# Kernel tuning notes

Hardware: AMD Instinct MI355X
Metric: run time of the kernel (lower is better)

Reference implementation:

```python
import jax, jax.numpy as jnp
import numpy as np

N, E, L = 50000, 800000, 3
EPS = 1e-5


def mlp2(h, W1, b1, W2, b2):
    # Linear -> ReLU -> Linear
    return jax.nn.relu(h @ W1 + b1) @ W2 + b2


def setup_inputs() -> dict:
    key = jax.random.key(0)
    ks = jax.random.split(key, 20)
    s = 0.1  # weight scale to keep activations well-conditioned
    return {
        "x": jax.random.normal(ks[0], (N, 128), jnp.float32),
        "edge_attr": jax.random.normal(ks[1], (E, 64), jnp.float32),
        "edge_index": jax.random.randint(ks[2], (2, E), 0, N, dtype=jnp.int32),
        "Wn1": jax.random.normal(ks[3], (L, 128, 256), jnp.float32) * s,
        "bn1": jnp.zeros((L, 256), jnp.float32),
        "Wn2": jax.random.normal(ks[4], (L, 256, 128), jnp.float32) * s,
        "bn2": jnp.zeros((L, 128), jnp.float32),
        "We1": jax.random.normal(ks[5], (L, 64, 128), jnp.float32) * s,
        "be1": jnp.zeros((L, 128), jnp.float32),
        "We2": jax.random.normal(ks[6], (L, 128, 64), jnp.float32) * s,
        "be2": jnp.zeros((L, 64), jnp.float32),
        "Wm1": jax.random.normal(ks[7], (L, 320, 128), jnp.float32) * s,
        "bm1": jnp.zeros((L, 128), jnp.float32),
        "Wm2": jax.random.normal(ks[8], (L, 128, 128), jnp.float32) * s,
        "bm2": jnp.zeros((L, 128), jnp.float32),
        "lnw": jnp.ones((L, 128), jnp.float32),
        "lnb": jnp.zeros((L, 128), jnp.float32),
        "Wf": jax.random.normal(ks[9], (128, 64), jnp.float32) * s,
        "bf": jnp.zeros((64,), jnp.float32),
    }


def reference(x, edge_attr, edge_index, Wn1, bn1, Wn2, bn2, We1, be1, We2, be2,
              Wm1, bm1, Wm2, bm2, lnw, lnb, Wf, bf):
    src, dst = edge_index[0], edge_index[1]  # x_j = x[src], x_i = x[dst] (PyG source_to_target)
    deg = jax.ops.segment_sum(jnp.ones((E,), x.dtype), dst, num_segments=N)
    denom = jnp.maximum(deg, 1.0)[:, None]  # scatter-mean with clamp for isolated nodes
    for l in range(L):
        # mlp_node is the same function for x_i and x_j -> apply once per node, then gather
        xn = mlp2(x, Wn1[l], bn1[l], Wn2[l], bn2[l])        # [N, 128]
        e = mlp2(edge_attr, We1[l], be1[l], We2[l], be2[l])  # [E, 64]
        m = jnp.concatenate([xn[dst], xn[src], e], axis=-1)  # [E, 320] = [x_i, x_j, edge_attr]
        m = mlp2(m, Wm1[l], bm1[l], Wm2[l], bm2[l])          # [E, 128]
        agg = jax.ops.segment_sum(m, dst, num_segments=N) / denom  # mean aggregate [N, 128]
        mu = agg.mean(-1, keepdims=True)
        var = agg.var(-1, keepdims=True)
        h = (agg - mu) * jax.lax.rsqrt(var + EPS) * lnw[l] + lnb[l]  # LayerNorm
        x = jax.nn.relu(h)  # dropout p=0.0 -> identity
    return x @ Wf + bf  # jk='last' -> final linear on last layer output
```

## Files before the change

### kernel.cpp

```cpp
#include <hip/hip_runtime.h>
#include <stdint.h>

#define NN 50000
#define NE 800000
#define NB 196

typedef float f32x4 __attribute__((ext_vector_type(4)));
typedef short bf16x8 __attribute__((ext_vector_type(8)));

__device__ __forceinline__ unsigned short f2bf(float f) {
  union { float f; unsigned u; } v; v.f = f;
  unsigned r = v.u + 0x7fffu + ((v.u >> 16) & 1u);
  return (unsigned short)(r >> 16);
}
__device__ __forceinline__ float bf2f(unsigned short h) {
  union { unsigned u; float f; } v; v.u = ((unsigned)h) << 16;
  return v.f;
}
__device__ __forceinline__ float ldf(const void* p, size_t i, int m32) {
  return m32 ? ((const float*)p)[i] : bf2f(((const unsigned short*)p)[i]);
}

__global__ void detect_kernel(const void* lnw, int* flag) {
  if (threadIdx.x == 0 && blockIdx.x == 0)
    *flag = (((const unsigned short*)lnw)[0] == 0x3F80) ? 0 : 1;
}

#define oWn1 0
#define oWn2 98304
#define oWm1 196608
#define oWe1 319488
#define oWe2 344064
#define oWm2 368640
#define oWf  417792
#define NWTOT 425984
#define obn1 0
#define obn2 768
#define obe1 1152
#define obe2 1536
#define obm1 1728
#define obm2 2112
#define olnw 2496
#define olnb 2880
#define obf  3264
#define NBTOT 3328

__global__ __launch_bounds__(256) void conv_w(
    const void* Wn1, const void* Wn2, const void* Wm1, const void* We1,
    const void* We2, const void* Wm2, const void* Wf,
    const int* __restrict__ flg, unsigned short* __restrict__ cW)
{
  const int m32 = *flg;
  int i = blockIdx.x * 256 + threadIdx.x;
  if (i >= NWTOT) return;
  const void* src; size_t j;
  if      (i < oWn2) { src = Wn1; j = i - oWn1; }
  else if (i < oWm1) { src = Wn2; j = i - oWn2; }
  else if (i < oWe1) { src = Wm1; j = i - oWm1; }
  else if (i < oWe2) { src = We1; j = i - oWe1; }
  else if (i < oWm2) { src = We2; j = i - oWe2; }
  else if (i < oWf)  { src = Wm2; j = i - oWm2; }
  else               { src = Wf;  j = i - oWf;  }
  cW[i] = f2bf(ldf(src, j, m32));
}

__global__ __launch_bounds__(256) void conv_b(
    const void* bn1, const void* bn2, const void* be1, const void* be2,
    const void* bm1, const void* bm2, const void* lnw, const void* lnb,
    const void* bfv, const int* __restrict__ flg, float* __restrict__ cB)
{
  const int m32 = *flg;
  int i = blockIdx.x * 256 + threadIdx.x;
  if (i >= NBTOT) return;
  const void* src; size_t j;
  if      (i < obn2) { src = bn1; j = i - obn1; }
  else if (i < obe1) { src = bn2; j = i - obn2; }
  else if (i < obe2) { src = be1; j = i - obe1; }
  else if (i < obm1) { src = be2; j = i - obe2; }
  else if (i < obm2) { src = bm1; j = i - obm1; }
  else if (i < olnw) { src = bm2; j = i - obm2; }
  else if (i < olnb) { src = lnw; j = i - olnw; }
  else if (i < obf)  { src = lnb; j = i - olnb; }
  else               { src = bfv; j = i - obf;  }
  cB[i] = ldf(src, j, m32);
}

__global__ __launch_bounds__(256) void conv_x(const void* x, const int* flg,
                                              unsigned short* xc) {
  const int m32 = *flg;
  size_t i = (size_t)blockIdx.x * 256 + threadIdx.x;
  if (i < (size_t)NN * 128) xc[i] = f2bf(ldf(x, i, m32));
}

__global__ __launch_bounds__(256) void deg_int(const int* __restrict__ eidx,
                                               int* __restrict__ degi) {
  int i = blockIdx.x * 256 + threadIdx.x;
  if (i < NE) atomicAdd(degi + eidx[NE + i], 1);
}

__global__ __launch_bounds__(256) void scan1(const int* __restrict__ degi,
                                             int* __restrict__ base,
                                             int* __restrict__ bsum) {
  __shared__ int s[256];
  int t = threadIdx.x, i = blockIdx.x * 256 + t;
  int v = (i < NN) ? degi[i] : 0;
  s[t] = v; __syncthreads();
  for (int d = 1; d < 256; d <<= 1) {
    int u = (t >= d) ? s[t - d] : 0;
    __syncthreads();
    s[t] += u;
    __syncthreads();
  }
  if (i < NN) base[i] = s[t] - v;
  if (t == 255) bsum[blockIdx.x] = s[255];
}

__global__ void scan2(int* bsum) {
  __shared__ int s[256];
  int t = threadIdx.x;
  int v = (t < NB) ? bsum[t] : 0;
  s[t] = v; __syncthreads();
  for (int d = 1; d < 256; d <<= 1) {
    int u = (t >= d) ? s[t - d] : 0;
    __syncthreads();
    s[t] += u;
    __syncthreads();
  }
  if (t < NB) bsum[t] = s[t] - v;
}

__global__ __launch_bounds__(256) void scan3(int* base, const int* bsum) {
  int i = blockIdx.x * 256 + threadIdx.x;
  if (i < NN) base[i] += bsum[blockIdx.x];
}

__global__ __launch_bounds__(256) void scatter_sort(
    const int* __restrict__ eidx, const int* __restrict__ base,
    int* __restrict__ cursor, int* __restrict__ sE,
    int* __restrict__ sSrc, int* __restrict__ sDst) {
  int e = blockIdx.x * 256 + threadIdx.x;
  if (e < NE) {
    int s = eidx[e], d = eidx[NE + e];
    int r = atomicAdd(cursor + d, 1);
    int pos = base[d] + r;
    sE[pos] = e; sSrc[pos] = s; sDst[pos] = d;
  }
}

__global__ __launch_bounds__(256) void gather_ea(
    const void* __restrict__ ea, const int* __restrict__ sE,
    const int* __restrict__ flg, unsigned short* __restrict__ eaS) {
  const int m32 = *flg;
  int slot = blockIdx.x * 32 + (threadIdx.x >> 3);
  int j = threadIdx.x & 7;
  if (slot >= NE) return;
  int eid = sE[slot];
  unsigned short* dst = eaS + (size_t)slot * 64 + j * 8;
  if (m32) {
    const float* src = (const float*)ea + (size_t)eid * 64 + j * 8;
    f32x4 v0 = *(const f32x4*)src;
    f32x4 v1 = *(const f32x4*)(src + 4);
    alignas(16) unsigned short t[8];
    #pragma unroll
    for (int q = 0; q < 4; q++) { t[q] = f2bf(v0[q]); t[4 + q] = f2bf(v1[q]); }
    *(bf16x8*)dst = *(const bf16x8*)t;
  } else {
    const unsigned short* src = (const unsigned short*)ea + (size_t)eid * 64 + j * 8;
    *(bf16x8*)dst = *(const bf16x8*)src;
  }
}

__global__ __launch_bounds__(256) void prep_wc(
    const unsigned short* __restrict__ cW, const float* __restrict__ cB,
    float* __restrict__ Wc, float* __restrict__ bc2)
{
  int l = blockIdx.x;
  const unsigned short* We2l = cW + oWe2 + l * 8192;
  const unsigned short* Wm1c = cW + oWm1 + l * 40960 + 256 * 128;
  const float* be2l = cB + obe2 + l * 64;
  const float* bm1l = cB + obm1 + l * 128;
  float* out = Wc + l * 16384;
  for (int i = threadIdx.x; i < 16384; i += 256) {
    int k = i >> 7, n = i & 127;
    float s = 0.f;
    for (int u = 0; u < 64; u++)
      s += bf2f(We2l[k * 64 + u]) * bf2f(Wm1c[u * 128 + n]);
    out[i] = s;
  }
  if (threadIdx.x < 128) {
    int n = threadIdx.x;
    float s = bm1l[n];
    for (int u = 0; u < 64; u++)
      s += bf2f(be2l[u]) * bf2f(Wm1c[u * 128 + n]);
    bc2[l * 128 + n] = s;
  }
}

__global__ __launch_bounds__(256) void pack_frags(
    const unsigned short* __restrict__ cW, const float* __restrict__ Wcp,
    unsigned short* __restrict__ Wn1p, unsigned short* __restrict__ Wn2p,
    unsigned short* __restrict__ Wm1p, unsigned short* __restrict__ We1p,
    unsigned short* __restrict__ Wcpk)
{
  int l = blockIdx.x / 5, which = blockIdx.x % 5;
  int K, N, total;
  const unsigned short* src = nullptr;
  const float* srcf = nullptr;
  unsigned short* dst;
  if (which == 0)      { K = 128; N = 256; src = cW + oWn1 + (size_t)l * 32768; dst = Wn1p + (size_t)l * 32768; }
  else if (which == 1) { K = 256; N = 128; src = cW + oWn2 + (size_t)l * 32768; dst = Wn2p + (size_t)l * 32768; }
  else if (which == 2) { K = 128; N = 256; src = cW + oWm1 + (size_t)l * 40960; dst = Wm1p + (size_t)l * 32768; }
  else if (which == 3) { K = 64;  N = 128; src = cW + oWe1 + (size_t)l * 8192;  dst = We1p + (size_t)l * 8192; }
  else                 { K = 128; N = 128; srcf = Wcp + (size_t)l * 16384;      dst = Wcpk + (size_t)l * 16384; }
  int KB = K >> 5;
  total = K * N;
  for (int o = threadIdx.x; o < total; o += 256) {
    int j = o & 7, lane = (o >> 3) & 63, q = o >> 9;
    int kb = q % KB, c = q / KB;
    int k = kb * 32 + (lane >> 4) * 8 + j;
    int n = c * 16 + (lane & 15);
    unsigned short v;
    if (which == 2) {
      v = (n < 128) ? src[k * 128 + n] : src[(128 + k) * 128 + (n - 128)];
    } else if (which == 4) {
      v = f2bf(srcf[k * 128 + n]);
    } else {
      v = src[k * N + n];
    }
    dst[o] = v;
  }
}

__global__ __launch_bounds__(256) void node_p_mfma(
    const unsigned short* __restrict__ xin,
    const unsigned short* __restrict__ Wn1p, const unsigned short* __restrict__ Wn2p,
    const unsigned short* __restrict__ Wm1p, const float* __restrict__ cB,
    unsigned short* __restrict__ P, int l)
{
  __shared__ __align__(16) short HS[4][16 * 256];
  const int tid = threadIdx.x;
  const int wid = tid >> 6, lane = tid & 63, rl = lane & 15, cg = lane >> 4;
  const int n0 = blockIdx.x * 64;
  short* Hw = &HS[wid][0];
  const int swr = (rl & 7) << 3;

  int nA = n0 + wid * 16 + rl;
  int nAc = (nA < NN) ? nA : (NN - 1);

  bf16x8 ax[4];
  {
    const unsigned short* xr = xin + (size_t)nAc * 128;
    #pragma unroll
    for (int kb = 0; kb < 4; kb++)
      ax[kb] = *(const bf16x8*)&xr[kb * 32 + cg * 8];
  }

  {
    const unsigned short* Wb = Wn1p + (size_t)l * 32768;
    const float* b1 = cB + obn1 + l * 256;
    #pragma unroll
    for (int c = 0; c < 16; c++) {
      f32x4 acc = {0.f, 0.f, 0.f, 0.f};
      #pragma unroll
      for (int kb = 0; kb < 4; kb++) {
        bf16x8 b = *(const bf16x8*)&Wb[(size_t)(c * 4 + kb) * 512 + lane * 8];
        acc = __builtin_amdgcn_mfma_f32_16x16x32_bf16(ax[kb], b, acc, 0, 0, 0);
      }
      int col = c * 16 + rl;
      float bb = b1[col];
      #pragma unroll
      for (int r = 0; r < 4; r++) {
        int row = cg * 4 + r;
        Hw[row * 256 + (col ^ ((row & 7) << 3))] =
            (short)f2bf(fmaxf(acc[r] + bb, 0.f));
      }
    }
  }

  {
    bf16x8 ah[8];
    #pragma unroll
    for (int kb = 0; kb < 8; kb++)
      ah[kb] = *(const bf16x8*)&Hw[rl * 256 + ((kb * 32 + cg * 8) ^ swr)];
    const unsigned short* Wb = Wn2p + (size_t)l * 32768;
    const float* b2 = cB + obn2 + l * 128;
    #pragma unroll
    for (int c = 0; c < 8; c++) {
      f32x4 acc = {0.f, 0.f, 0.f, 0.f};
      #pragma unroll
      for (int kb = 0; kb < 8; kb++) {
        bf16x8 b = *(const bf16x8*)&Wb[(size_t)(c * 8 + kb) * 512 + lane * 8];
        acc = __builtin_amdgcn_mfma_f32_16x16x32_bf16(ah[kb], b, acc, 0, 0, 0);
      }
      int col = c * 16 + rl;
      float bb = b2[col];
      #pragma unroll
      for (int r = 0; r < 4; r++) {
        int row = cg * 4 + r;
        Hw[row * 128 + (col ^ ((row & 7) << 3))] = (short)f2bf(acc[r] + bb);
      }
    }
  }

  {
    bf16x8 an[4];
    #pragma unroll
    for (int kb = 0; kb < 4; kb++)
      an[kb] = *(const bf16x8*)&Hw[rl * 128 + ((kb * 32 + cg * 8) ^ swr)];
    const unsigned short* Wb = Wm1p + (size_t)l * 32768;
    #pragma unroll
    for (int c = 0; c < 16; c++) {
      f32x4 acc = {0.f, 0.f, 0.f, 0.f};
      #pragma unroll
      for (int kb = 0; kb < 4; kb++) {
        bf16x8 b = *(const bf16x8*)&Wb[(size_t)(c * 4 + kb) * 512 + lane * 8];
        acc = __builtin_amdgcn_mfma_f32_16x16x32_bf16(an[kb], b, acc, 0, 0, 0);
      }
      int col = c * 16 + rl;
      #pragma unroll
      for (int r = 0; r < 4; r++) {
        int row = cg * 4 + r;
        int n = n0 + wid * 16 + row;
        if (n < NN) P[(size_t)n * 256 + col] = f2bf(acc[r]);
      }
    }
  }
}

__global__ __launch_bounds__(256, 8) void edge_fold_v4(
    const unsigned short* __restrict__ eaS,
    const int* __restrict__ sSrc, const int* __restrict__ sDst,
    const int* __restrict__ baseg, const int* __restrict__ degg,
    const unsigned short* __restrict__ We1p, const unsigned short* __restrict__ Wcpk,
    const float* __restrict__ cB, const float* __restrict__ bc2,
    const unsigned short* __restrict__ P, float* __restrict__ agg, int l)
{
  __shared__ __align__(16) short hS[64 * 136];
  __shared__ int dstS[64];
  const int tid = threadIdx.x;
  const int wid = tid >> 6, lane = tid & 63, rl = lane & 15, cg = lane >> 4;
  const int e0 = blockIdx.x * 64;
  short* Rw = hS + wid * 2048;
  const int swr = (rl & 7) << 3;
  const int brow = wid * 16 + rl;

  if (cg == 0) dstS[brow] = sDst[e0 + brow];

  int di[4], si[4];
  #pragma unroll
  for (int r = 0; r < 4; r++) {
    int row = e0 + wid * 16 + cg * 4 + r;
    di[r] = sDst[row];
    si[r] = sSrc[row];
  }

  const unsigned short* er = eaS + (size_t)(e0 + brow) * 64;
  bf16x8 a0 = *(const bf16x8*)&er[cg * 8];
  bf16x8 a1 = *(const bf16x8*)&er[32 + cg * 8];

  {
    const unsigned short* Wb = We1p + (size_t)l * 8192;
    const float* be1l = cB + obe1 + l * 128;
    #pragma unroll
    for (int c = 0; c < 8; c++) {
      bf16x8 b0 = *(const bf16x8*)&Wb[(c * 2 + 0) * 512 + lane * 8];
      bf16x8 b1 = *(const bf16x8*)&Wb[(c * 2 + 1) * 512 + lane * 8];
      f32x4 acc = {0.f, 0.f, 0.f, 0.f};
      acc = __builtin_amdgcn_mfma_f32_16x16x32_bf16(a0, b0, acc, 0, 0, 0);
      acc = __builtin_amdgcn_mfma_f32_16x16x32_bf16(a1, b1, acc, 0, 0, 0);
      int col = c * 16 + rl;
      float b = be1l[col];
      #pragma unroll
      for (int r = 0; r < 4; r++) {
        int row = cg * 4 + r;
        Rw[row * 128 + (col ^ ((row & 7) << 3))] =
            (short)f2bf(fmaxf(acc[r] + b, 0.f));
      }
    }
  }

  f32x4 acc2[8];
  {
    bf16x8 ra[4];
    #pragma unroll
    for (int kb = 0; kb < 4; kb++)
      ra[kb] = *(const bf16x8*)&Rw[rl * 128 + ((kb * 32 + cg * 8) ^ swr)];
    const unsigned short* Wb = Wcpk + (size_t)l * 16384;
    #pragma unroll
    for (int c = 0; c < 8; c++) {
      f32x4 acc = {0.f, 0.f, 0.f, 0.f};
      #pragma unroll
      for (int kb = 0; kb < 4; kb++) {
        bf16x8 b = *(const bf16x8*)&Wb[(c * 4 + kb) * 512 + lane * 8];
        acc = __builtin_amdgcn_mfma_f32_16x16x32_bf16(ra[kb], b, acc, 0, 0, 0);
      }
      acc2[c] = acc;
    }
  }

  __syncthreads();

  {
    const float* bc2l = bc2 + l * 128;
    #pragma unroll
    for (int c = 0; c < 8; c++) {
      int col = c * 16 + rl;
      float bv = bc2l[col];
      #pragma unroll
      for (int r = 0; r < 4; r++) {
        int row = wid * 16 + cg * 4 + r;
        float h = acc2[c][r] + bv
                + bf2f(P[(size_t)di[r] * 256 + col])
                + bf2f(P[(size_t)si[r] * 256 + 128 + col]);
        hS[row * 136 + col] = (short)f2bf(fmaxf(h, 0.f));
      }
    }
  }
  __syncthreads();

  if (tid < 128) {
    const int col = tid;
    float run = 0.f;
    int cur = dstS[0];
    for (int i = 0; i < 64; i++) {
      int d = dstS[i];
      if (d != cur) {
        int b0 = baseg[cur], dg = degg[cur];
        if (b0 >= e0 && b0 + dg <= e0 + 64)
          agg[(size_t)cur * 128 + col] = run;
        else
          atomicAdd(agg + (size_t)cur * 128 + col, run);
        run = 0.f; cur = d;
      }
      run += bf2f((unsigned short)hS[i * 136 + col]);
    }
    int b0 = baseg[cur], dg = degg[cur];
    if (b0 >= e0 && b0 + dg <= e0 + 64)
      agg[(size_t)cur * 128 + col] = run;
    else
      atomicAdd(agg + (size_t)cur * 128 + col, run);
  }
}

__global__ __launch_bounds__(256) void agg_w_ln(
    const float* __restrict__ aggH, const int* __restrict__ degi,
    const unsigned short* __restrict__ cW, const float* __restrict__ cB,
    unsigned short* __restrict__ xnext, int l)
{
  __shared__ float at[8][128];
  __shared__ float vs[8][128];
  const int tid = threadIdx.x;
  const int n0 = blockIdx.x * 8;
  for (int i = tid; i < 1024; i += 256) {
    int j = i >> 7, k = i & 127;
    int n = n0 + j;
    int d = degi[n];
    at[j][k] = aggH[(size_t)n * 128 + k] / (float)(d > 0 ? d : 1);
  }
  __syncthreads();
  {
    const int t = tid & 127, grp = tid >> 7;
    float acc[4] = {0.f, 0.f, 0.f, 0.f};
    const unsigned short* W = cW + oWm2 + (size_t)l * 16384 + t;
    for (int k = 0; k < 128; k += 4) {
      float w0 = bf2f(W[(k + 0) * 128]);
      float w1 = bf2f(W[(k + 1) * 128]);
      float w2 = bf2f(W[(k + 2) * 128]);
      float w3 = bf2f(W[(k + 3) * 128]);
      #pragma unroll
      for (int j = 0; j < 4; j++) {
        f32x4 v = *(const f32x4*)&at[grp * 4 + j][k];
        acc[j] += v[0] * w0 + v[1] * w1 + v[2] * w2 + v[3] * w3;
      }
    }
    float bm = cB[obm2 + l * 128 + t];
    #pragma unroll
    for (int j = 0; j < 4; j++) {
      int n = n0 + grp * 4 + j;
      vs[grp * 4 + j][t] = acc[j] + (degi[n] > 0 ? bm : 0.f);
    }
  }
  __syncthreads();
  const int w = tid >> 6, lane = tid & 63;
  float lw0 = cB[olnw + l * 128 + lane], lb0 = cB[olnb + l * 128 + lane];
  float lw1 = cB[olnw + l * 128 + lane + 64], lb1 = cB[olnb + l * 128 + lane + 64];
  #pragma unroll
  for (int jj = 0; jj < 2; jj++) {
    int j = w * 2 + jj;
    float v0 = vs[j][lane], v1 = vs[j][lane + 64];
    float s = v0 + v1, q = v0 * v0 + v1 * v1;
    #pragma unroll
    for (int m = 1; m < 64; m <<= 1) {
      s += __shfl_xor(s, m, 64);
      q += __shfl_xor(q, m, 64);
    }
    float mu = s * (1.f / 128.f);
    float var = fmaxf(q * (1.f / 128.f) - mu * mu, 0.f);
    float rs = rsqrtf(var + 1e-5f);
    int n = n0 + j;
    xnext[(size_t)n * 128 + lane] = f2bf(fmaxf((v0 - mu) * rs * lw0 + lb0, 0.f));
    xnext[(size_t)n * 128 + lane + 64] = f2bf(fmaxf((v1 - mu) * rs * lw1 + lb1, 0.f));
  }
}

__global__ __launch_bounds__(256) void final_k(
    const unsigned short* __restrict__ xc, const unsigned short* __restrict__ cW,
    const float* __restrict__ cB, const int* __restrict__ flg,
    void* __restrict__ out)
{
  const int m32 = *flg;
  const int tid = threadIdx.x;
  const int t = tid & 63;
  const int nd = blockIdx.x * 4 + (tid >> 6);
  float acc = cB[obf + t];
  const unsigned short* xr = xc + (size_t)nd * 128;
  const unsigned short* W = cW + oWf + t;
  for (int k = 0; k < 128; k++)
    acc += bf2f(xr[k]) * bf2f(W[(size_t)k * 64]);
  if (m32) ((float*)out)[(size_t)nd * 64 + t] = acc;
  else ((unsigned short*)out)[(size_t)nd * 64 + t] = f2bf(acc);
}

extern "C" void kernel_launch(void* const* d_in, const int* in_sizes, int n_in,
                              void* d_out, int out_size, void* d_ws, size_t ws_size,
                              hipStream_t stream) {
  (void)in_sizes; (void)n_in; (void)out_size; (void)ws_size;
  const void* x    = d_in[0];
  const void* ea   = d_in[1];
  const int*  eidx = (const int*)d_in[2];
  const void* Wn1  = d_in[3];
  const void* bn1  = d_in[4];
  const void* Wn2  = d_in[5];
  const void* bn2  = d_in[6];
  const void* We1  = d_in[7];
  const void* be1  = d_in[8];
  const void* We2  = d_in[9];
  const void* be2  = d_in[10];
  const void* Wm1  = d_in[11];
  const void* bm1  = d_in[12];
  const void* Wm2  = d_in[13];
  const void* bm2  = d_in[14];
  const void* lnw  = d_in[15];
  const void* lnb  = d_in[16];
  const void* Wf   = d_in[17];
  const void* bfv  = d_in[18];

  char* ws = (char*)d_ws;
  size_t off = 0;
  auto alloc = [&](size_t bytes) {
    size_t o = off;
    off += (bytes + 255) & ~(size_t)255;
    return o;
  };
  int*            flag = (int*)(ws + alloc(4));
  unsigned short* xcur = (unsigned short*)(ws + alloc((size_t)NN * 128 * 2));
  unsigned short* Pb   = (unsigned short*)(ws + alloc((size_t)NN * 256 * 2));
  float*          aggH = (float*)(ws + alloc((size_t)NN * 128 * 4));
  unsigned short* cW   = (unsigned short*)(ws + alloc((size_t)NWTOT * 2));
  float*          cB   = (float*)(ws + alloc((size_t)NBTOT * 4));
  float*          Wcp  = (float*)(ws + alloc(3 * 16384 * 4));
  float*          bc2w = (float*)(ws + alloc(3 * 128 * 4));
  unsigned short* We1p = (unsigned short*)(ws + alloc(3 * 8192 * 2));
  unsigned short* Wcpk = (unsigned short*)(ws + alloc(3 * 16384 * 2));
  unsigned short* Wn1p = (unsigned short*)(ws + alloc(3 * 32768 * 2));
  unsigned short* Wn2p = (unsigned short*)(ws + alloc(3 * 32768 * 2));
  unsigned short* Wm1p = (unsigned short*)(ws + alloc(3 * 32768 * 2));
  int*            degi = (int*)(ws + alloc((size_t)NN * 4));
  int*            baseb= (int*)(ws + alloc((size_t)NN * 4));
  int*            bsum = (int*)(ws + alloc(256 * 4));
  int*            curs = (int*)(ws + alloc((size_t)NN * 4));
  int*            sE   = (int*)(ws + alloc((size_t)NE * 4));
  int*            sSrc = (int*)(ws + alloc((size_t)NE * 4));
  int*            sDst = (int*)(ws + alloc((size_t)NE * 4));
  unsigned short* eaS  = (unsigned short*)(ws + alloc((size_t)NE * 64 * 2));

  detect_kernel<<<1, 64, 0, stream>>>(lnw, flag);
  conv_w<<<(NWTOT + 255) / 256, 256, 0, stream>>>(Wn1, Wn2, Wm1, We1, We2, Wm2,
                                                  Wf, flag, cW);
  conv_b<<<(NBTOT + 255) / 256, 256, 0, stream>>>(bn1, bn2, be1, be2, bm1, bm2,
                                                  lnw, lnb, bfv, flag, cB);
  conv_x<<<(NN * 128 + 255) / 256, 256, 0, stream>>>(x, flag, xcur);

  hipMemsetAsync(degi, 0, (size_t)NN * 4, stream);
  deg_int<<<(NE + 255) / 256, 256, 0, stream>>>(eidx, degi);
  scan1<<<NB, 256, 0, stream>>>(degi, baseb, bsum);
  scan2<<<1, 256, 0, stream>>>(bsum);
  scan3<<<NB, 256, 0, stream>>>(baseb, bsum);
  hipMemsetAsync(curs, 0, (size_t)NN * 4, stream);
  scatter_sort<<<(NE + 255) / 256, 256, 0, stream>>>(eidx, baseb, curs, sE,
                                                     sSrc, sDst);
  gather_ea<<<NE / 32, 256, 0, stream>>>(ea, sE, flag, eaS);

  prep_wc<<<3, 256, 0, stream>>>(cW, cB, Wcp, bc2w);
  pack_frags<<<15, 256, 0, stream>>>(cW, Wcp, Wn1p, Wn2p, Wm1p, We1p, Wcpk);

  for (int l = 0; l < 3; l++) {
    node_p_mfma<<<(NN + 63) / 64, 256, 0, stream>>>(xcur, Wn1p, Wn2p, Wm1p,
                                                    cB, Pb, l);
    hipMemsetAsync(aggH, 0, (size_t)NN * 128 * 4, stream);
    edge_fold_v4<<<NE / 64, 256, 0, stream>>>(eaS, sSrc, sDst, baseb, degi,
                                              We1p, Wcpk, cB, bc2w, Pb,
                                              aggH, l);
    agg_w_ln<<<NN / 8, 256, 0, stream>>>(aggH, degi, cW, cB, xcur, l);
  }
  final_k<<<NN / 4, 256, 0, stream>>>(xcur, cW, cB, flag, d_out);
}
```

Measured before the change: 1.548 ms.

## Vectorize P gathers and stores, move aggregate Wm2+LayerNorm to MFMA

Three changes. The edge kernel now loads P rows with 16-byte vector gathers per edge instead of scalar bf16 loads per element, staging the partial result in swizzled LDS. The node projection kernel writes P through LDS as coalesced 16-byte row stores. The aggregate/Wm2/LayerNorm kernel is rewritten to use bf16 MFMA with packed Wm2 fragments, 64 nodes per block and vectorized output stores. The aim is to cut uncoalesced memory traffic and the scalar FMA cost, at the price of extra LDS passes and syncs and bf16 rounding of the aggregate before Wm2.

After: 1.525 ms. Within noise of the previous version (-1.5%).

```diff
diff --git a/kernel.cpp b/kernel.cpp
--- a/kernel.cpp
+++ b/kernel.cpp
@@ -200,9 +200,9 @@
     const unsigned short* __restrict__ cW, const float* __restrict__ Wcp,
     unsigned short* __restrict__ Wn1p, unsigned short* __restrict__ Wn2p,
     unsigned short* __restrict__ Wm1p, unsigned short* __restrict__ We1p,
-    unsigned short* __restrict__ Wcpk)
-{
-  int l = blockIdx.x / 5, which = blockIdx.x % 5;
+    unsigned short* __restrict__ Wcpk, unsigned short* __restrict__ Wm2p)
+{
+  int l = blockIdx.x / 6, which = blockIdx.x % 6;
   int K, N, total;
   const unsigned short* src = nullptr;
   const float* srcf = nullptr;
@@ -211,7 +211,8 @@
   else if (which == 1) { K = 256; N = 128; src = cW + oWn2 + (size_t)l * 32768; dst = Wn2p + (size_t)l * 32768; }
   else if (which == 2) { K = 128; N = 256; src = cW + oWm1 + (size_t)l * 40960; dst = Wm1p + (size_t)l * 32768; }
   else if (which == 3) { K = 64;  N = 128; src = cW + oWe1 + (size_t)l * 8192;  dst = We1p + (size_t)l * 8192; }
-  else                 { K = 128; N = 128; srcf = Wcp + (size_t)l * 16384;      dst = Wcpk + (size_t)l * 16384; }
+  else if (which == 4) { K = 128; N = 128; srcf = Wcp + (size_t)l * 16384;      dst = Wcpk + (size_t)l * 16384; }
+  else                 { K = 128; N = 128; src = cW + oWm2 + (size_t)l * 16384; dst = Wm2p + (size_t)l * 16384; }
   int KB = K >> 5;
   total = K * N;
   for (int o = threadIdx.x; o < total; o += 256) {
@@ -320,14 +321,27 @@
       #pragma unroll
       for (int r = 0; r < 4; r++) {
         int row = cg * 4 + r;
-        int n = n0 + wid * 16 + row;
-        if (n < NN) P[(size_t)n * 256 + col] = f2bf(acc[r]);
-      }
-    }
-  }
-}
-
-__global__ __launch_bounds__(256, 8) void edge_fold_v4(
+        Hw[row * 256 + (col ^ ((row & 7) << 3))] = (short)f2bf(acc[r]);
+      }
+    }
+  }
+  {
+    int row = lane >> 2;
+    int ch = (lane & 3) * 64;
+    int n = n0 + wid * 16 + row;
+    if (n < NN) {
+      int sw = (row & 7) << 3;
+      unsigned short* dst = P + (size_t)n * 256 + ch;
+      #pragma unroll
+      for (int g = 0; g < 8; g++) {
+        bf16x8 v = *(const bf16x8*)&Hw[row * 256 + ((ch + g * 8) ^ sw)];
+        *(bf16x8*)(dst + g * 8) = v;
+      }
+    }
+  }
+}
+
+__global__ __launch_bounds__(256, 8) void edge_fold_v5(
     const unsigned short* __restrict__ eaS,
     const int* __restrict__ sSrc, const int* __restrict__ sDst,
     const int* __restrict__ baseg, const int* __restrict__ degg,
@@ -336,7 +350,7 @@
     const unsigned short* __restrict__ P, float* __restrict__ agg, int l)
 {
   __shared__ __align__(16) short hS[64 * 136];
-  __shared__ int dstS[64];
+  __shared__ int dstS[64], srcS[64];
   const int tid = threadIdx.x;
   const int wid = tid >> 6, lane = tid & 63, rl = lane & 15, cg = lane >> 4;
   const int e0 = blockIdx.x * 64;
@@ -344,14 +358,9 @@
   const int swr = (rl & 7) << 3;
   const int brow = wid * 16 + rl;
 
-  if (cg == 0) dstS[brow] = sDst[e0 + brow];
-
-  int di[4], si[4];
-  #pragma unroll
-  for (int r = 0; r < 4; r++) {
-    int row = e0 + wid * 16 + cg * 4 + r;
-    di[r] = sDst[row];
-    si[r] = sSrc[row];
+  if (cg == 0) {
+    dstS[brow] = sDst[e0 + brow];
+    srcS[brow] = sSrc[e0 + brow];
   }
 
   const unsigned short* er = eaS + (size_t)(e0 + brow) * 64;
@@ -409,11 +418,34 @@
       #pragma unroll
       for (int r = 0; r < 4; r++) {
         int row = wid * 16 + cg * 4 + r;
-        float h = acc2[c][r] + bv
-                + bf2f(P[(size_t)di[r] * 256 + col])
-                + bf2f(P[(size_t)si[r] * 256 + 128 + col]);
-        hS[row * 136 + col] = (short)f2bf(fmaxf(h, 0.f));
-      }
+        hS[row * 136 + (col ^ ((row & 7) << 3))] =
+            (short)f2bf(acc2[c][r] + bv);
+      }
+    }
+  }
+  __syncthreads();
+
+  {
+    int row = tid & 63;
+    int ch = (tid >> 6) * 32;
+    int di = dstS[row], si = srcS[row];
+    int sw = (row & 7) << 3;
+    const unsigned short* Pd = P + (size_t)di * 256 + ch;
+    const unsigned short* Ps = P + (size_t)si * 256 + 128 + ch;
+    #pragma unroll
+    for (int g = 0; g < 4; g++) {
+      bf16x8 pd = *(const bf16x8*)(Pd + g * 8);
+      bf16x8 ps = *(const bf16x8*)(Ps + g * 8);
+      short* hp = &hS[row * 136 + ((ch + g * 8) ^ sw)];
+      bf16x8 hv = *(const bf16x8*)hp;
+      alignas(16) unsigned short o[8];
+      #pragma unroll
+      for (int j = 0; j < 8; j++) {
+        float h = bf2f((unsigned short)hv[j]) + bf2f((unsigned short)pd[j]) +
+                  bf2f((unsigned short)ps[j]);
+        o[j] = f2bf(fmaxf(h, 0.f));
+      }
+      *(bf16x8*)hp = *(const bf16x8*)o;
     }
   }
   __syncthreads();
@@ -432,7 +464,7 @@
           atomicAdd(agg + (size_t)cur * 128 + col, run);
         run = 0.f; cur = d;
       }
-      run += bf2f((unsigned short)hS[i * 136 + col]);
+      run += bf2f((unsigned short)hS[i * 136 + (col ^ ((i & 7) << 3))]);
     }
     int b0 = baseg[cur], dg = degg[cur];
     if (b0 >= e0 && b0 + dg <= e0 + 64)
@@ -442,64 +474,98 @@
   }
 }
 
-__global__ __launch_bounds__(256) void agg_w_ln(
+__global__ __launch_bounds__(256, 8) void agg_ln_mfma(
     const float* __restrict__ aggH, const int* __restrict__ degi,
-    const unsigned short* __restrict__ cW, const float* __restrict__ cB,
+    const unsigned short* __restrict__ Wm2p, const float* __restrict__ cB,
     unsigned short* __restrict__ xnext, int l)
 {
-  __shared__ float at[8][128];
-  __shared__ float vs[8][128];
+  __shared__ __align__(16) short OS[4][16 * 136];
   const int tid = threadIdx.x;
-  const int n0 = blockIdx.x * 8;
-  for (int i = tid; i < 1024; i += 256) {
-    int j = i >> 7, k = i & 127;
-    int n = n0 + j;
-    int d = degi[n];
-    at[j][k] = aggH[(size_t)n * 128 + k] / (float)(d > 0 ? d : 1);
-  }
-  __syncthreads();
-  {
-    const int t = tid & 127, grp = tid >> 7;
-    float acc[4] = {0.f, 0.f, 0.f, 0.f};
-    const unsigned short* W = cW + oWm2 + (size_t)l * 16384 + t;
-    for (int k = 0; k < 128; k += 4) {
-      float w0 = bf2f(W[(k + 0) * 128]);
-      float w1 = bf2f(W[(k + 1) * 128]);
-      float w2 = bf2f(W[(k + 2) * 128]);
-      float w3 = bf2f(W[(k + 3) * 128]);
-      #pragma unroll
-      for (int j = 0; j < 4; j++) {
-        f32x4 v = *(const f32x4*)&at[grp * 4 + j][k];
-        acc[j] += v[0] * w0 + v[1] * w1 + v[2] * w2 + v[3] * w3;
-      }
-    }
-    float bm = cB[obm2 + l * 128 + t];
-    #pragma unroll
-    for (int j = 0; j < 4; j++) {
-      int n = n0 + grp * 4 + j;
-      vs[grp * 4 + j][t] = acc[j] + (degi[n] > 0 ? bm : 0.f);
-    }
-  }
-  __syncthreads();
-  const int w = tid >> 6, lane = tid & 63;
-  float lw0 = cB[olnw + l * 128 + lane], lb0 = cB[olnb + l * 128 + lane];
-  float lw1 = cB[olnw + l * 128 + lane + 64], lb1 = cB[olnb + l * 128 + lane + 64];
+  const int wid = tid >> 6, lane = tid & 63, rl = lane & 15, cg = lane >> 4;
+  const int n0 = blockIdx.x * 64;
+  short* Ow = &OS[wid][0];
+
+  int nA = n0 + wid * 16 + rl;
+  int nAc = (nA < NN) ? nA : (NN - 1);
+  int dA = degi[nAc];
+  float degf = (float)dA;
+  float invd = 1.f / (float)(dA > 0 ? dA : 1);
+
+  bf16x8 af[4];
+  {
+    const float* ar = aggH + (size_t)nAc * 128;
+    #pragma unroll
+    for (int kb = 0; kb < 4; kb++) {
+      f32x4 v0 = *(const f32x4*)&ar[kb * 32 + cg * 8];
+      f32x4 v1 = *(const f32x4*)&ar[kb * 32 + cg * 8 + 4];
+      alignas(16) unsigned short t[8];
+      #pragma unroll
+      for (int q = 0; q < 4; q++) {
+        t[q] = f2bf(v0[q] * invd);
+        t[4 + q] = f2bf(v1[q] * invd);
+      }
+      af[kb] = *(const bf16x8*)t;
+    }
+  }
+
+  f32x4 acc[8];
+  {
+    const unsigned short* Wb = Wm2p + (size_t)l * 16384;
+    #pragma unroll
+    for (int c = 0; c < 8; c++) {
+      f32x4 a = {0.f, 0.f, 0.f, 0.f};
+      #pragma unroll
+      for (int kb = 0; kb < 4; kb++) {
+        bf16x8 b = *(const bf16x8*)&Wb[(c * 4 + kb) * 512 + lane * 8];
+        a = __builtin_amdgcn_mfma_f32_16x16x32_bf16(af[kb], b, a, 0, 0, 0);
+      }
+      acc[c] = a;
+    }
+  }
+
+  const float* bm2p = cB + obm2 + l * 128;
+  const float* lnwp = cB + olnw + l * 128;
+  const float* lnbp = cB + olnb + l * 128;
   #pragma unroll
-  for (int jj = 0; jj < 2; jj++) {
-    int j = w * 2 + jj;
-    float v0 = vs[j][lane], v1 = vs[j][lane + 64];
-    float s = v0 + v1, q = v0 * v0 + v1 * v1;
-    #pragma unroll
-    for (int m = 1; m < 64; m <<= 1) {
+  for (int r = 0; r < 4; r++) {
+    int row = cg * 4 + r;
+    float dg = __shfl(degf, row, 64);
+    float bmask = (dg > 0.f) ? 1.f : 0.f;
+    float v[8];
+    float s = 0.f, q = 0.f;
+    #pragma unroll
+    for (int c = 0; c < 8; c++) {
+      float x = acc[c][r] + bmask * bm2p[c * 16 + rl];
+      v[c] = x; s += x; q += x * x;
+    }
+    #pragma unroll
+    for (int m = 1; m < 16; m <<= 1) {
       s += __shfl_xor(s, m, 64);
       q += __shfl_xor(q, m, 64);
     }
     float mu = s * (1.f / 128.f);
     float var = fmaxf(q * (1.f / 128.f) - mu * mu, 0.f);
     float rs = rsqrtf(var + 1e-5f);
-    int n = n0 + j;
-    xnext[(size_t)n * 128 + lane] = f2bf(fmaxf((v0 - mu) * rs * lw0 + lb0, 0.f));
-    xnext[(size_t)n * 128 + lane + 64] = f2bf(fmaxf((v1 - mu) * rs * lw1 + lb1, 0.f));
+    #pragma unroll
+    for (int c = 0; c < 8; c++) {
+      int col = c * 16 + rl;
+      float y = fmaxf((v[c] - mu) * rs * lnwp[col] + lnbp[col], 0.f);
+      Ow[row * 136 + (col ^ ((row & 7) << 3))] = (short)f2bf(y);
+    }
+  }
+  {
+    int row = lane >> 2;
+    int ch = (lane & 3) * 32;
+    int n = n0 + wid * 16 + row;
+    if (n < NN) {
+      int sw = (row & 7) << 3;
+      unsigned short* dst = xnext + (size_t)n * 128 + ch;
+      #pragma unroll
+      for (int g = 0; g < 4; g++) {
+        bf16x8 v = *(const bf16x8*)&Ow[row * 136 + ((ch + g * 8) ^ sw)];
+        *(bf16x8*)(dst + g * 8) = v;
+      }
+    }
   }
 }
 
@@ -565,6 +631,7 @@
   unsigned short* Wn1p = (unsigned short*)(ws + alloc(3 * 32768 * 2));
   unsigned short* Wn2p = (unsigned short*)(ws + alloc(3 * 32768 * 2));
   unsigned short* Wm1p = (unsigned short*)(ws + alloc(3 * 32768 * 2));
+  unsigned short* Wm2p = (unsigned short*)(ws + alloc(3 * 16384 * 2));
   int*            degi = (int*)(ws + alloc((size_t)NN * 4));
   int*            baseb= (int*)(ws + alloc((size_t)NN * 4));
   int*            bsum = (int*)(ws + alloc(256 * 4));
@@ -592,16 +659,18 @@
   gather_ea<<<NE / 32, 256, 0, stream>>>(ea, sE, flag, eaS);
 
   prep_wc<<<3, 256, 0, stream>>>(cW, cB, Wcp, bc2w);
-  pack_frags<<<15, 256, 0, stream>>>(cW, Wcp, Wn1p, Wn2p, Wm1p, We1p, Wcpk);
+  pack_frags<<<18, 256, 0, stream>>>(cW, Wcp, Wn1p, Wn2p, Wm1p, We1p, Wcpk,
+                                     Wm2p);
 
   for (int l = 0; l < 3; l++) {
     node_p_mfma<<<(NN + 63) / 64, 256, 0, stream>>>(xcur, Wn1p, Wn2p, Wm1p,
                                                     cB, Pb, l);
     hipMemsetAsync(aggH, 0, (size_t)NN * 128 * 4, stream);
-    edge_fold_v4<<<NE / 64, 256, 0, stream>>>(eaS, sSrc, sDst, baseb, degi,
+    edge_fold_v5<<<NE / 64, 256, 0, stream>>>(eaS, sSrc, sDst, baseb, degi,
                                               We1p, Wcpk, cB, bc2w, Pb,
                                               aggH, l);
-    agg_w_ln<<<NN / 8, 256, 0, stream>>>(aggH, degi, cW, cB, xcur, l);
+    agg_ln_mfma<<<(NN + 63) / 64, 256, 0, stream>>>(aggH, degi, Wm2p, cB,
+                                                    xcur, l);
   }
   final_k<<<NN / 4, 256, 0, stream>>>(xcur, cW, cB, flag, d_out);
 }
```
